# Optimization experiments

Measured on AMD Instinct MI355X. Metric: run time of the kernel, lower is better.

## Reference

```python
import jax, jax.numpy as jnp
import numpy as np

N = 40000   # number of points
K = 32      # neighbors per point (fixed-degree CSR for synthetic indices)
C = 256     # embed_dim
H = 8       # num_heads
HD = C // H # head_dim = 32
M = N * K   # number of (query, key) pairs


def setup_inputs() -> dict:
    key = jax.random.key(0)
    ks = jax.random.split(key, 12)
    s = 1.0 / np.sqrt(C).astype(np.float32)
    query_feats = jax.random.normal(ks[0], (N, C), jnp.float32)
    Wq = jax.random.normal(ks[1], (C, C), jnp.float32) * s
    bq = jax.random.normal(ks[2], (C,), jnp.float32) * 0.01
    Wk = jax.random.normal(ks[3], (C, C), jnp.float32) * s
    bk = jax.random.normal(ks[4], (C,), jnp.float32) * 0.01
    Wv = jax.random.normal(ks[5], (C, C), jnp.float32) * s
    bv = jax.random.normal(ks[6], (C,), jnp.float32) * 0.01
    Wp = jax.random.normal(ks[7], (C, C), jnp.float32) * s
    bp = jax.random.normal(ks[8], (C,), jnp.float32) * 0.01
    # CSR pair lists: index_0 sorted (K pairs per query point), index_1 = neighbor ids
    index_0 = jnp.repeat(jnp.arange(N, dtype=jnp.int32), K)
    index_1 = jax.random.randint(ks[9], (M,), 0, N, dtype=jnp.int32)
    sort_idx = jax.random.permutation(ks[10], N).astype(jnp.int32)
    return dict(query_feats=query_feats, Wq=Wq, bq=bq, Wk=Wk, bk=bk, Wv=Wv, bv=bv,
                Wp=Wp, bp=bp, index_0=index_0, index_1=index_1, sort_idx=sort_idx)


def reference(query_feats, Wq, bq, Wk, bk, Wv, bv, Wp, bp, index_0, index_1, sort_idx):
    # pe_type='none', attntion_type='qkv', key=value=query (self-attention), dropout=0
    scale = HD ** -0.5
    q = ((query_feats @ Wq) + bq).reshape(N, H, HD) * scale
    k = ((query_feats @ Wk) + bk).reshape(N, H, HD)
    v = ((query_feats @ Wv) + bv).reshape(N, H, HD)
    # sort into window-contiguous order
    qs = q[sort_idx]
    ks_ = k[sort_idx]
    vs = v[sort_idx]
    # attention_step1: per-pair QK dot over head_dim -> (M, H)
    attn = jnp.einsum('mhd,mhd->mh', qs[index_0], ks_[index_1])
    # scatter_softmax_csr over variable-length neighbor segments (grouped by index_0)
    seg_max = jax.ops.segment_max(attn, index_0, num_segments=N, indices_are_sorted=True)
    e = jnp.exp(attn - seg_max[index_0])
    seg_sum = jax.ops.segment_sum(e, index_0, num_segments=N, indices_are_sorted=True)
    p = e / seg_sum[index_0]  # (M, H)
    # attention_step2: weighted value gather + segment reduce -> (N, H, HD)
    xs = jax.ops.segment_sum(p[:, :, None] * vs[index_1], index_0,
                             num_segments=N, indices_are_sorted=True)
    # scatter back to original order: out[sort_idx] = xs
    x = jnp.zeros((N, C), query_feats.dtype).at[sort_idx].set(xs.reshape(N, C))
    # output projection
    return x @ Wp + bp
```

## Files before the change

### kernel.cpp

```cpp
#include <hip/hip_runtime.h>
#include <hip/hip_bf16.h>

#define NPTS 40000
#define KNBR 32
#define CDIM 256
#define NH 8
#define HD 32

static constexpr float QK_SCALE = 0.17677669529663687f;

typedef __attribute__((ext_vector_type(8))) __bf16 bf16x8;
typedef __attribute__((ext_vector_type(4))) __bf16 bf16x4;
typedef __attribute__((ext_vector_type(4))) float f32x4;

static __device__ __forceinline__ unsigned int bfbits(float f) {
    __bf16 h = (__bf16)f;
    union { __bf16 b; unsigned short u; } c; c.b = h;
    return (unsigned int)c.u;
}

__global__ __launch_bounds__(256) void wtr_kernel(
    const float* __restrict__ W0, const float* __restrict__ W1,
    const float* __restrict__ W2, const float* __restrict__ W3,
    __bf16* __restrict__ T0, __bf16* __restrict__ T1,
    __bf16* __restrict__ T2, __bf16* __restrict__ T3)
{
    __shared__ float tile[32][33];
    const float* Ws[4] = {W0, W1, W2, W3};
    __bf16* Ts[4] = {T0, T1, T2, T3};
    const float* W = Ws[blockIdx.z];
    __bf16* Wt = Ts[blockIdx.z];
    const int t = threadIdx.x;
    const int k0 = blockIdx.x * 32, n0 = blockIdx.y * 32;
    const int r = t >> 3, c4 = (t & 7) * 4;
    const float4 v = *reinterpret_cast<const float4*>(&W[(k0 + r) * CDIM + n0 + c4]);
    tile[r][c4 + 0] = v.x; tile[r][c4 + 1] = v.y;
    tile[r][c4 + 2] = v.z; tile[r][c4 + 3] = v.w;
    __syncthreads();
    __bf16 o[4];
    #pragma unroll
    for (int i = 0; i < 4; ++i) o[i] = (__bf16)tile[c4 + i][r];
    *reinterpret_cast<ulong1*>(&Wt[(n0 + r) * CDIM + k0 + c4]) =
        *reinterpret_cast<ulong1*>(o);
}

static __device__ __forceinline__ void mfma_pass(
    const __bf16 xb[64][272], const __bf16* __restrict__ Wt,
    int lr, int lk, int nbase, f32x4 acc[4][4])
{
    #pragma unroll
    for (int mf = 0; mf < 4; ++mf)
        #pragma unroll
        for (int nf = 0; nf < 4; ++nf)
            acc[mf][nf] = (f32x4){0.f, 0.f, 0.f, 0.f};

    #pragma unroll 2
    for (int k0 = 0; k0 < CDIM; k0 += 32) {
        bf16x8 a[4];
        #pragma unroll
        for (int mf = 0; mf < 4; ++mf)
            a[mf] = *reinterpret_cast<const bf16x8*>(&xb[mf * 16 + lr][k0 + lk]);
        #pragma unroll
        for (int nf = 0; nf < 4; ++nf) {
            const bf16x8 b = *reinterpret_cast<const bf16x8*>(
                Wt + (size_t)(nbase + nf * 16 + lr) * CDIM + k0 + lk);
            #pragma unroll
            for (int mf = 0; mf < 4; ++mf)
                acc[mf][nf] = __builtin_amdgcn_mfma_f32_16x16x32_bf16(a[mf], b, acc[mf][nf], 0, 0, 0);
        }
    }
}

__global__ __launch_bounds__(256, 2) void qkv_kernel(
    const float* __restrict__ X, const int* __restrict__ sort_idx,
    const __bf16* __restrict__ WtQ, const __bf16* __restrict__ WtK, const __bf16* __restrict__ WtV,
    const float* __restrict__ bq, const float* __restrict__ bk, const float* __restrict__ bv,
    __bf16* __restrict__ qs, unsigned int* __restrict__ kvs)
{
    __shared__ __bf16 xb[64][272];
    const int t = threadIdx.x;
    const int row0 = blockIdx.x * 64;

    #pragma unroll 8
    for (int r = 0; r < 64; ++r) {
        const int src = sort_idx[row0 + r];
        xb[r][t] = (__bf16)X[(size_t)src * CDIM + t];
    }
    __syncthreads();

    const int w = t >> 6, l = t & 63;
    const int lr = l & 15;
    const int lk = (l >> 4) * 8;
    const int nbase = w * 64;
    const int rbase = (l >> 4) * 4;

    f32x4 acc[4][4];
    unsigned int kp[4][4][2];

    mfma_pass(xb, WtK, lr, lk, nbase, acc);
    #pragma unroll
    for (int nf = 0; nf < 4; ++nf) {
        const float bkv = bk[nbase + nf * 16 + lr];
        #pragma unroll
        for (int mf = 0; mf < 4; ++mf)
            #pragma unroll
            for (int p = 0; p < 2; ++p)
                kp[nf][mf][p] = bfbits(acc[mf][nf][2 * p] + bkv) |
                                (bfbits(acc[mf][nf][2 * p + 1] + bkv) << 16);
    }

    mfma_pass(xb, WtV, lr, lk, nbase, acc);
    #pragma unroll
    for (int nf = 0; nf < 4; ++nf) {
        const int col = nbase + nf * 16 + lr;
        const float bvv = bv[col];
        #pragma unroll
        for (int mf = 0; mf < 4; ++mf) {
            #pragma unroll
            for (int i = 0; i < 4; ++i) {
                const int row = row0 + mf * 16 + rbase + i;
                const unsigned int kb = (kp[nf][mf][i >> 1] >> (16 * (i & 1))) & 0xffffu;
                const unsigned int vb = bfbits(acc[mf][nf][i] + bvv);
                kvs[(size_t)row * CDIM + col] = kb | (vb << 16);
            }
        }
    }

    mfma_pass(xb, WtQ, lr, lk, nbase, acc);
    #pragma unroll
    for (int nf = 0; nf < 4; ++nf) {
        const int col = nbase + nf * 16 + lr;
        const float bqv = bq[col];
        #pragma unroll
        for (int mf = 0; mf < 4; ++mf) {
            #pragma unroll
            for (int i = 0; i < 4; ++i) {
                const int row = row0 + mf * 16 + rbase + i;
                qs[(size_t)row * CDIM + col] = (__bf16)((acc[mf][nf][i] + bqv) * QK_SCALE);
            }
        }
    }
}

__global__ __launch_bounds__(256, 8) void attn_kernel(
    const __bf16* __restrict__ qs, const unsigned int* __restrict__ kvs,
    const int* __restrict__ index_1, const int* __restrict__ sort_idx,
    __bf16* __restrict__ xbuf)
{
    const int wv = __builtin_amdgcn_readfirstlane(threadIdx.x) >> 6;
    const int n = blockIdx.x * 4 + wv;
    const int l = threadIdx.x & 63;
    const int c0 = l * 4;

    const bf16x4 qv4 = *reinterpret_cast<const bf16x4*>(&qs[(size_t)n * CDIM + c0]);
    const float qx = (float)qv4[0], qy = (float)qv4[1];
    const float qz = (float)qv4[2], qw = (float)qv4[3];
    float lsum = 0.f;
    float o0 = 0.f, o1 = 0.f, o2 = 0.f, o3 = 0.f;
    const int* idx = index_1 + (size_t)n * KNBR;

    #pragma unroll 4
    for (int j = 0; j < KNBR; ++j) {
        const int nb = idx[j];
        const uint4 kv = *reinterpret_cast<const uint4*>(&kvs[(size_t)nb * CDIM + c0]);
        const float k0 = __uint_as_float(kv.x << 16);
        const float v0 = __uint_as_float(kv.x & 0xffff0000u);
        const float k1 = __uint_as_float(kv.y << 16);
        const float v1 = __uint_as_float(kv.y & 0xffff0000u);
        const float k2 = __uint_as_float(kv.z << 16);
        const float v2 = __uint_as_float(kv.z & 0xffff0000u);
        const float k3 = __uint_as_float(kv.w << 16);
        const float v3 = __uint_as_float(kv.w & 0xffff0000u);
        float dot = qx * k0;
        dot = fmaf(qy, k1, dot);
        dot = fmaf(qz, k2, dot);
        dot = fmaf(qw, k3, dot);
        dot += __shfl_xor(dot, 1);
        dot += __shfl_xor(dot, 2);
        dot += __shfl_xor(dot, 4);
        const float e = __expf(dot);
        lsum += e;
        o0 = fmaf(e, v0, o0);
        o1 = fmaf(e, v1, o1);
        o2 = fmaf(e, v2, o2);
        o3 = fmaf(e, v3, o3);
    }

    const float inv = 1.f / lsum;
    const int orig = sort_idx[n];
    __bf16 o[4];
    o[0] = (__bf16)(o0 * inv); o[1] = (__bf16)(o1 * inv);
    o[2] = (__bf16)(o2 * inv); o[3] = (__bf16)(o3 * inv);
    *reinterpret_cast<ulong1*>(&xbuf[(size_t)orig * CDIM + c0]) =
        *reinterpret_cast<ulong1*>(o);
}

__global__ __launch_bounds__(256, 2) void proj_kernel(
    const __bf16* __restrict__ X, const __bf16* __restrict__ WtP, const float* __restrict__ bp,
    float* __restrict__ out)
{
    const int t = threadIdx.x;
    const int w = t >> 6, l = t & 63;
    const int row0 = blockIdx.x * 64;
    const int lr = l & 15;
    const int lk = (l >> 4) * 8;
    const int nbase = w * 64;
    const int rbase = (l >> 4) * 4;

    const __bf16* pA[4];
    #pragma unroll
    for (int mf = 0; mf < 4; ++mf)
        pA[mf] = X + (size_t)(row0 + mf * 16 + lr) * CDIM + lk;

    f32x4 acc[4][4];
    #pragma unroll
    for (int mf = 0; mf < 4; ++mf)
        #pragma unroll
        for (int nf = 0; nf < 4; ++nf)
            acc[mf][nf] = (f32x4){0.f, 0.f, 0.f, 0.f};

    #pragma unroll 2
    for (int k0 = 0; k0 < CDIM; k0 += 32) {
        bf16x8 a[4];
        #pragma unroll
        for (int mf = 0; mf < 4; ++mf)
            a[mf] = *reinterpret_cast<const bf16x8*>(pA[mf] + k0);
        #pragma unroll
        for (int nf = 0; nf < 4; ++nf) {
            const bf16x8 b = *reinterpret_cast<const bf16x8*>(
                WtP + (size_t)(nbase + nf * 16 + lr) * CDIM + k0 + lk);
            #pragma unroll
            for (int mf = 0; mf < 4; ++mf)
                acc[mf][nf] = __builtin_amdgcn_mfma_f32_16x16x32_bf16(a[mf], b, acc[mf][nf], 0, 0, 0);
        }
    }

    #pragma unroll
    for (int nf = 0; nf < 4; ++nf) {
        const int col = nbase + nf * 16 + lr;
        const float bpv = bp[col];
        #pragma unroll
        for (int mf = 0; mf < 4; ++mf) {
            #pragma unroll
            for (int i = 0; i < 4; ++i) {
                const int row = row0 + mf * 16 + rbase + i;
                out[(size_t)row * CDIM + col] = acc[mf][nf][i] + bpv;
            }
        }
    }
}

extern "C" void kernel_launch(void* const* d_in, const int* in_sizes, int n_in,
                              void* d_out, int out_size, void* d_ws, size_t ws_size,
                              hipStream_t stream) {
    const float* qf  = (const float*)d_in[0];
    const float* Wq  = (const float*)d_in[1];
    const float* bq  = (const float*)d_in[2];
    const float* Wk  = (const float*)d_in[3];
    const float* bk  = (const float*)d_in[4];
    const float* Wv  = (const float*)d_in[5];
    const float* bv  = (const float*)d_in[6];
    const float* Wp  = (const float*)d_in[7];
    const float* bp  = (const float*)d_in[8];
    const int* index_1  = (const int*)d_in[10];
    const int* sort_idx = (const int*)d_in[11];
    float* out = (float*)d_out;

    __bf16* qs = (__bf16*)d_ws;
    unsigned int* kvs = (unsigned int*)(qs + (size_t)NPTS * CDIM);
    __bf16* xbuf = (__bf16*)(kvs + (size_t)NPTS * CDIM);
    __bf16* WtQ = xbuf + (size_t)NPTS * CDIM;
    __bf16* WtK = WtQ + CDIM * CDIM;
    __bf16* WtV = WtK + CDIM * CDIM;
    __bf16* WtP = WtV + CDIM * CDIM;

    wtr_kernel<<<dim3(8, 8, 4), 256, 0, stream>>>(Wq, Wk, Wv, Wp, WtQ, WtK, WtV, WtP);
    qkv_kernel<<<NPTS / 64, 256, 0, stream>>>(qf, sort_idx, WtQ, WtK, WtV, bq, bk, bv, qs, kvs);
    attn_kernel<<<NPTS / 4, 256, 0, stream>>>(qs, kvs, index_1, sort_idx, xbuf);
    proj_kernel<<<NPTS / 64, 256, 0, stream>>>(xbuf, WtP, bp, out);
}
```

Measured before the change: 264.9 us.

## Fuse attention and output projection into one kernel via LDS tile

Merges the attention and output projection kernels. Each block computes attention for 16 query points into a shared-memory tile, then runs the projection MFMA on that tile and scatters the rows to the original order. This removes the xbuf round trip through global memory and one kernel launch. In exchange, each block reloads the full WtP matrix (more L2 traffic across 2500 blocks), adds a block barrier, and lowers occupancy.

```diff
diff --git a/kernel.cpp b/kernel.cpp
--- a/kernel.cpp
+++ b/kernel.cpp
@@ -142,111 +142,95 @@
     }
 }
 
-__global__ __launch_bounds__(256, 8) void attn_kernel(
+__global__ __launch_bounds__(256, 4) void attnproj_kernel(
     const __bf16* __restrict__ qs, const unsigned int* __restrict__ kvs,
     const int* __restrict__ index_1, const int* __restrict__ sort_idx,
-    __bf16* __restrict__ xbuf)
-{
+    const __bf16* __restrict__ WtP, const float* __restrict__ bp,
+    float* __restrict__ out)
+{
+    __shared__ __bf16 xt[16][272];
     const int wv = __builtin_amdgcn_readfirstlane(threadIdx.x) >> 6;
-    const int n = blockIdx.x * 4 + wv;
     const int l = threadIdx.x & 63;
     const int c0 = l * 4;
-
-    const bf16x4 qv4 = *reinterpret_cast<const bf16x4*>(&qs[(size_t)n * CDIM + c0]);
-    const float qx = (float)qv4[0], qy = (float)qv4[1];
-    const float qz = (float)qv4[2], qw = (float)qv4[3];
-    float lsum = 0.f;
-    float o0 = 0.f, o1 = 0.f, o2 = 0.f, o3 = 0.f;
-    const int* idx = index_1 + (size_t)n * KNBR;
-
-    #pragma unroll 4
-    for (int j = 0; j < KNBR; ++j) {
-        const int nb = idx[j];
-        const uint4 kv = *reinterpret_cast<const uint4*>(&kvs[(size_t)nb * CDIM + c0]);
-        const float k0 = __uint_as_float(kv.x << 16);
-        const float v0 = __uint_as_float(kv.x & 0xffff0000u);
-        const float k1 = __uint_as_float(kv.y << 16);
-        const float v1 = __uint_as_float(kv.y & 0xffff0000u);
-        const float k2 = __uint_as_float(kv.z << 16);
-        const float v2 = __uint_as_float(kv.z & 0xffff0000u);
-        const float k3 = __uint_as_float(kv.w << 16);
-        const float v3 = __uint_as_float(kv.w & 0xffff0000u);
-        float dot = qx * k0;
-        dot = fmaf(qy, k1, dot);
-        dot = fmaf(qz, k2, dot);
-        dot = fmaf(qw, k3, dot);
-        dot += __shfl_xor(dot, 1);
-        dot += __shfl_xor(dot, 2);
-        dot += __shfl_xor(dot, 4);
-        const float e = __expf(dot);
-        lsum += e;
-        o0 = fmaf(e, v0, o0);
-        o1 = fmaf(e, v1, o1);
-        o2 = fmaf(e, v2, o2);
-        o3 = fmaf(e, v3, o3);
-    }
-
-    const float inv = 1.f / lsum;
-    const int orig = sort_idx[n];
-    __bf16 o[4];
-    o[0] = (__bf16)(o0 * inv); o[1] = (__bf16)(o1 * inv);
-    o[2] = (__bf16)(o2 * inv); o[3] = (__bf16)(o3 * inv);
-    *reinterpret_cast<ulong1*>(&xbuf[(size_t)orig * CDIM + c0]) =
-        *reinterpret_cast<ulong1*>(o);
-}
-
-__global__ __launch_bounds__(256, 2) void proj_kernel(
-    const __bf16* __restrict__ X, const __bf16* __restrict__ WtP, const float* __restrict__ bp,
-    float* __restrict__ out)
-{
-    const int t = threadIdx.x;
-    const int w = t >> 6, l = t & 63;
-    const int row0 = blockIdx.x * 64;
+    const int q0 = blockIdx.x * 16;
+
+    #pragma unroll
+    for (int qq = 0; qq < 4; ++qq) {
+        const int n = q0 + wv * 4 + qq;
+        const bf16x4 qv4 = *reinterpret_cast<const bf16x4*>(&qs[(size_t)n * CDIM + c0]);
+        const float qx = (float)qv4[0], qy = (float)qv4[1];
+        const float qz = (float)qv4[2], qw = (float)qv4[3];
+        float lsum = 0.f;
+        float o0 = 0.f, o1 = 0.f, o2 = 0.f, o3 = 0.f;
+        const int* idx = index_1 + (size_t)n * KNBR;
+
+        #pragma unroll 4
+        for (int j = 0; j < KNBR; ++j) {
+            const int nb = idx[j];
+            const uint4 kv = *reinterpret_cast<const uint4*>(&kvs[(size_t)nb * CDIM + c0]);
+            const float k0 = __uint_as_float(kv.x << 16);
+            const float v0 = __uint_as_float(kv.x & 0xffff0000u);
+            const float k1 = __uint_as_float(kv.y << 16);
+            const float v1 = __uint_as_float(kv.y & 0xffff0000u);
+            const float k2 = __uint_as_float(kv.z << 16);
+            const float v2 = __uint_as_float(kv.z & 0xffff0000u);
+            const float k3 = __uint_as_float(kv.w << 16);
+            const float v3 = __uint_as_float(kv.w & 0xffff0000u);
+            float dot = qx * k0;
+            dot = fmaf(qy, k1, dot);
+            dot = fmaf(qz, k2, dot);
+            dot = fmaf(qw, k3, dot);
+            dot += __shfl_xor(dot, 1);
+            dot += __shfl_xor(dot, 2);
+            dot += __shfl_xor(dot, 4);
+            const float e = __expf(dot);
+            lsum += e;
+            o0 = fmaf(e, v0, o0);
+            o1 = fmaf(e, v1, o1);
+            o2 = fmaf(e, v2, o2);
+            o3 = fmaf(e, v3, o3);
+        }
+
+        const float inv = 1.f / lsum;
+        __bf16 o[4];
+        o[0] = (__bf16)(o0 * inv); o[1] = (__bf16)(o1 * inv);
+        o[2] = (__bf16)(o2 * inv); o[3] = (__bf16)(o3 * inv);
+        *reinterpret_cast<ulong1*>(&xt[wv * 4 + qq][c0]) =
+            *reinterpret_cast<ulong1*>(o);
+    }
+    __syncthreads();
+
     const int lr = l & 15;
     const int lk = (l >> 4) * 8;
-    const int nbase = w * 64;
+    const int nbase = wv * 64;
     const int rbase = (l >> 4) * 4;
 
-    const __bf16* pA[4];
-    #pragma unroll
-    for (int mf = 0; mf < 4; ++mf)
-        pA[mf] = X + (size_t)(row0 + mf * 16 + lr) * CDIM + lk;
-
-    f32x4 acc[4][4];
-    #pragma unroll
-    for (int mf = 0; mf < 4; ++mf)
-        #pragma unroll
-        for (int nf = 0; nf < 4; ++nf)
-            acc[mf][nf] = (f32x4){0.f, 0.f, 0.f, 0.f};
+    f32x4 acc[4];
+    #pragma unroll
+    for (int nf = 0; nf < 4; ++nf) acc[nf] = (f32x4){0.f, 0.f, 0.f, 0.f};
 
     #pragma unroll 2
     for (int k0 = 0; k0 < CDIM; k0 += 32) {
-        bf16x8 a[4];
-        #pragma unroll
-        for (int mf = 0; mf < 4; ++mf)
-            a[mf] = *reinterpret_cast<const bf16x8*>(pA[mf] + k0);
+        const bf16x8 a = *reinterpret_cast<const bf16x8*>(&xt[lr][k0 + lk]);
         #pragma unroll
         for (int nf = 0; nf < 4; ++nf) {
             const bf16x8 b = *reinterpret_cast<const bf16x8*>(
                 WtP + (size_t)(nbase + nf * 16 + lr) * CDIM + k0 + lk);
-            #pragma unroll
-            for (int mf = 0; mf < 4; ++mf)
-                acc[mf][nf] = __builtin_amdgcn_mfma_f32_16x16x32_bf16(a[mf], b, acc[mf][nf], 0, 0, 0);
-        }
-    }
+            acc[nf] = __builtin_amdgcn_mfma_f32_16x16x32_bf16(a, b, acc[nf], 0, 0, 0);
+        }
+    }
+
+    int srow[4];
+    #pragma unroll
+    for (int i = 0; i < 4; ++i) srow[i] = sort_idx[q0 + rbase + i];
 
     #pragma unroll
     for (int nf = 0; nf < 4; ++nf) {
         const int col = nbase + nf * 16 + lr;
         const float bpv = bp[col];
         #pragma unroll
-        for (int mf = 0; mf < 4; ++mf) {
-            #pragma unroll
-            for (int i = 0; i < 4; ++i) {
-                const int row = row0 + mf * 16 + rbase + i;
-                out[(size_t)row * CDIM + col] = acc[mf][nf][i] + bpv;
-            }
-        }
+        for (int i = 0; i < 4; ++i)
+            out[(size_t)srow[i] * CDIM + col] = acc[nf][i] + bpv;
     }
 }
 
@@ -268,14 +252,12 @@
 
     __bf16* qs = (__bf16*)d_ws;
     unsigned int* kvs = (unsigned int*)(qs + (size_t)NPTS * CDIM);
-    __bf16* xbuf = (__bf16*)(kvs + (size_t)NPTS * CDIM);
-    __bf16* WtQ = xbuf + (size_t)NPTS * CDIM;
+    __bf16* WtQ = (__bf16*)(kvs + (size_t)NPTS * CDIM);
     __bf16* WtK = WtQ + CDIM * CDIM;
     __bf16* WtV = WtK + CDIM * CDIM;
     __bf16* WtP = WtV + CDIM * CDIM;
 
     wtr_kernel<<<dim3(8, 8, 4), 256, 0, stream>>>(Wq, Wk, Wv, Wp, WtQ, WtK, WtV, WtP);
     qkv_kernel<<<NPTS / 64, 256, 0, stream>>>(qf, sort_idx, WtQ, WtK, WtV, bq, bk, bv, qs, kvs);
-    attn_kernel<<<NPTS / 4, 256, 0, stream>>>(qs, kvs, index_1, sort_idx, xbuf);
-    proj_kernel<<<NPTS / 64, 256, 0, stream>>>(xbuf, WtP, bp, out);
-}
+    attnproj_kernel<<<NPTS / 16, 256, 0, stream>>>(qs, kvs, index_1, sort_idx, WtP, bp, out);
+}
```

Measured after the change: 241.3 us. 8.9% less time.
